# Performance work log

Measured on AMD Instinct MI355X. Metric: run time of the kernel, lower is better.

## Reference

```python
import jax, jax.numpy as jnp
from jax import lax
import numpy as np

B, T, D_IN, H, L, D_OUT = 1024, 512, 6, 128, 3, 1


def _lstm_layer(xs, w_ih, w_hh, b_ih, b_hh):
    """xs: [B, T, Din]; w_ih: [4H, Din]; w_hh: [4H, H]. PyTorch gate order i,f,g,o."""
    Bq = xs.shape[0]
    Hq = w_hh.shape[1]
    # Precompute the input projection for all timesteps (compute-dense part).
    x_proj = jnp.einsum('btd,gd->btg', xs, w_ih) + (b_ih + b_hh)  # [B, T, 4H]

    def step(carry, xp):
        h, c = carry
        gates = xp + h @ w_hh.T  # [B, 4H]
        i, f, g, o = jnp.split(gates, 4, axis=-1)
        i = jax.nn.sigmoid(i)
        f = jax.nn.sigmoid(f)
        g = jnp.tanh(g)
        o = jax.nn.sigmoid(o)
        c = f * c + i * g
        h = o * jnp.tanh(c)
        return (h, c), h

    h0 = jnp.zeros((Bq, Hq), xs.dtype)
    c0 = jnp.zeros((Bq, Hq), xs.dtype)
    (_, _), hs = lax.scan(step, (h0, c0), jnp.swapaxes(x_proj, 0, 1))  # hs: [T, B, H]
    return jnp.swapaxes(hs, 0, 1)  # [B, T, H]


def setup_inputs() -> dict:
    key = jax.random.key(0)
    ks = jax.random.split(key, 16)
    s = 1.0 / np.sqrt(H)  # PyTorch LSTM init scale
    inp = {"x": jax.random.normal(ks[0], (B, T, D_IN), dtype=jnp.float32)}
    din = D_IN
    for l in range(L):
        inp[f"w_ih{l}"] = jax.random.uniform(ks[1 + 4 * l], (4 * H, din), minval=-s, maxval=s, dtype=jnp.float32)
        inp[f"w_hh{l}"] = jax.random.uniform(ks[2 + 4 * l], (4 * H, H), minval=-s, maxval=s, dtype=jnp.float32)
        inp[f"b_ih{l}"] = jax.random.uniform(ks[3 + 4 * l], (4 * H,), minval=-s, maxval=s, dtype=jnp.float32)
        inp[f"b_hh{l}"] = jax.random.uniform(ks[4 + 4 * l], (4 * H,), minval=-s, maxval=s, dtype=jnp.float32)
        din = H
    inp["fc_w"] = jax.random.uniform(ks[13], (D_OUT, H), minval=-s, maxval=s, dtype=jnp.float32)
    inp["fc_b"] = jax.random.uniform(ks[14], (D_OUT,), minval=-s, maxval=s, dtype=jnp.float32)
    return inp


def reference(x, w_ih0, w_hh0, b_ih0, b_hh0, w_ih1, w_hh1, b_ih1, b_hh1,
              w_ih2, w_hh2, b_ih2, b_hh2, fc_w, fc_b):
    # 3-layer LSTM (inference: dropout between layers is identity) + final Linear on last timestep.
    h = _lstm_layer(x, w_ih0, w_hh0, b_ih0, b_hh0)
    h = _lstm_layer(h, w_ih1, w_hh1, b_ih1, b_hh1)
    h = _lstm_layer(h, w_ih2, w_hh2, b_ih2, b_hh2)
    return h[:, -1, :] @ fc_w.T + fc_b  # [B, 1]
```

## Files before the change

kernel.cpp:

```cpp
#include <hip/hip_runtime.h>

#define TLEN  512
#define HID   128
#define RSLOT 16

typedef __attribute__((ext_vector_type(8))) short          bf16x8;
typedef __attribute__((ext_vector_type(4))) float          f32x4;
typedef __attribute__((ext_vector_type(4))) unsigned short u16x4;
typedef unsigned long long u64;

#define LOG2E  1.4426950408889634f
#define LOG2E2 2.8853900817779268f

template<bool B> struct BC { static constexpr bool value = B; };

__device__ __forceinline__ unsigned short f2bf(float f) {
    union { float f; unsigned u; } v; v.f = f;
    unsigned r = v.u + 0x7fffu + ((v.u >> 16) & 1u);
    return (unsigned short)(r >> 16);
}
__device__ __forceinline__ unsigned short f2bf_fast(float f) {
    union { float f; unsigned u; } v; v.f = f;
    return (unsigned short)((v.u + 0x8000u) >> 16);
}

__device__ __forceinline__ float sig_ps(float xs) {
    return __builtin_amdgcn_rcpf(1.0f + __builtin_exp2f(-xs));
}
__device__ __forceinline__ float tanh_ps(float xs) {
    return 2.0f * __builtin_amdgcn_rcpf(1.0f + __builtin_exp2f(-xs)) - 1.0f;
}


__device__ __forceinline__ int flag_peek(const int* f) {
    return __hip_atomic_load(f, __ATOMIC_RELAXED, __HIP_MEMORY_SCOPE_AGENT);
}
__device__ __forceinline__ int flag_spin(const int* f, int v) {
    int x = flag_peek(f);
    while (x < v) { __builtin_amdgcn_s_sleep(1); x = flag_peek(f); }
    return x;
}
__device__ __forceinline__ void flag_pub(int* f, int v) {
    __hip_atomic_store(f, v, __ATOMIC_RELAXED, __HIP_MEMORY_SCOPE_WORKGROUP);
}

template<int MODE, bool CONS, bool PROD, bool WFC>
__device__ __forceinline__ void run_layer_p(
    const float* __restrict__ xin,
    const u64* __restrict__ rin, u64* __restrict__ rout,
    const int* pin_flag, int* cout_flag, const int* cin_flag, int* pout_flag,
    const float* __restrict__ wih, const float* __restrict__ whh,
    const float* __restrict__ bih, const float* __restrict__ bhh,
    unsigned short (* __restrict__ hbuf)[2048],
    unsigned short (* __restrict__ xbuf)[2048],
    float* __restrict__ fcred,
    const int tid, const int wave, const int lane,
    const int n16, const int quad, const int bbase)
{
    constexpr int NKTX = MODE ? 4 : 1;
    constexpr int DINL = MODE ? 128 : 6;

    bf16x8 Wfx[4][NKTX], Wfh[4][4];
    float  bb[4];
#pragma unroll
    for (int g = 0; g < 4; ++g) {
        const float sc = (g == 2) ? LOG2E2 : LOG2E;
        const int row = g * 128 + wave * 16 + n16;
        bb[g] = (bih[row] + bhh[row]) * sc;
#pragma unroll
        for (int kt = 0; kt < NKTX; ++kt) {
            bf16x8 wv;
#pragma unroll
            for (int j = 0; j < 8; ++j) {
                const int k = kt * 32 + quad * 8 + j;
                wv[j] = (short)f2bf(((k < DINL) ? wih[row * DINL + k] : 0.0f) * sc);
            }
            Wfx[g][kt] = wv;
        }
#pragma unroll
        for (int kt = 0; kt < 4; ++kt) {
            bf16x8 wv;
#pragma unroll
            for (int j = 0; j < 8; ++j) {
                const int k = kt * 32 + quad * 8 + j;
                wv[j] = (short)f2bf(whh[row * HID + k] * sc);
            }
            Wfh[g][kt] = wv;
        }
    }

    const int rof  = (lane ^ quad) * 8;
    const int j    = wave * 16 + n16;
    const int beta = ((j & 31) >> 3) & 3;
    const int wbase = ((j >> 5) * 64 + ((j & 31) >> 3) * 16 + quad * 4) * 8 + (j & 7);
    int wof[4];
#pragma unroll
    for (int r = 0; r < 4; ++r) wof[r] = wbase + ((r ^ beta) * 8);
    const int uof  = ((((tid >> 1) ^ ((tid >> 5) & 3))) << 3) + (tid & 1) * 4;
    const int xm = tid >> 5, xk = tid & 31;
    const int eiS = ((xk >> 3) * 16 + (xm ^ (xk >> 3))) * 8 + (xk & 7);

    { u16x4 z = {0, 0, 0, 0}; *(u16x4*)&hbuf[0][uof] = z; }
    u64 q0 = 0, q1 = 0, q2 = 0, qn = 0;
    float pfx0 = 0.0f;
    int pend = 0, cpend = 0;
    if constexpr (CONS) {
        flag_spin(pin_flag, 1);
        *(u64*)&xbuf[0][uof] =
            __hip_atomic_load(rin + tid, __ATOMIC_RELAXED, __HIP_MEMORY_SCOPE_AGENT);
        flag_spin(pin_flag, 2);
        *(u64*)&xbuf[1][uof] =
            __hip_atomic_load(rin + 512 + tid, __ATOMIC_RELAXED, __HIP_MEMORY_SCOPE_AGENT);
        pend = flag_spin(pin_flag, 5);
        q0 = __hip_atomic_load(rin + 2 * 512 + tid, __ATOMIC_RELAXED, __HIP_MEMORY_SCOPE_AGENT);
        q1 = __hip_atomic_load(rin + 3 * 512 + tid, __ATOMIC_RELAXED, __HIP_MEMORY_SCOPE_AGENT);
        q2 = __hip_atomic_load(rin + 4 * 512 + tid, __ATOMIC_RELAXED, __HIP_MEMORY_SCOPE_AGENT);
    } else {
        float v0 = (xk < DINL) ? xin[((bbase + xm) * TLEN + 0) * DINL + xk] : 0.0f;
        float v1 = (xk < DINL) ? xin[((bbase + xm) * TLEN + 1) * DINL + xk] : 0.0f;
        xbuf[0][eiS] = f2bf(v0);
        xbuf[1][eiS] = f2bf(v1);
        if (xk < DINL) pfx0 = xin[((bbase + xm) * TLEN + 2) * DINL + xk];
    }
    if constexpr (PROD) cpend = -(1 << 30);
    __syncthreads();

    f32x4 accA[4], accB[4];
#pragma unroll
    for (int g = 0; g < 4; ++g) { f32x4 bi = {bb[g], bb[g], bb[g], bb[g]}; accA[g] = bi; }
#pragma unroll
    for (int kt = 0; kt < NKTX; ++kt) {
        bf16x8 a = *(const bf16x8*)&xbuf[0][rof + kt * 512];
#pragma unroll
        for (int g = 0; g < 4; ++g)
            accA[g] = __builtin_amdgcn_mfma_f32_16x16x32_bf16(a, Wfx[g][kt], accA[g], 0, 0, 0);
    }

    float cst[4] = {0.f, 0.f, 0.f, 0.f};
    float hf[4];
    int rd = 1, wr = 2;

    auto step = [&](auto SHc, auto CMc, f32x4 (&accC)[4], f32x4 (&accN)[4], int t) {
        constexpr bool SH = decltype(SHc)::value;
        constexpr bool CM = decltype(CMc)::value;
        const int cur = t & 1, nxt = cur ^ 1;
        __syncthreads();

        const unsigned short* __restrict__ hcur = hbuf[cur];
        const unsigned short* __restrict__ xrd  = xbuf[rd];

        bf16x8 ha_[4];
#pragma unroll
        for (int kt = 0; kt < 4; ++kt) ha_[kt] = *(const bf16x8*)&hcur[rof + kt * 512];

        if constexpr (CONS) {
            if (t + 5 < TLEN) {
                if (pend < t + 6) pend = flag_spin(pin_flag, t + 6);
                qn = __hip_atomic_load(rin + ((t + 5) & (RSLOT - 1)) * 512 + tid,
                                       __ATOMIC_RELAXED, __HIP_MEMORY_SCOPE_AGENT);
                pend = flag_peek(pin_flag);
            }
        }
        if (tid == 0) {
            if constexpr (CONS) if ((t & 3) == 0) flag_pub(cout_flag, t + 5);
            if constexpr (PROD) if (t >= 2)       flag_pub(pout_flag, t - 1);
        }
        if constexpr (PROD) {
            if (t >= 1) {
                const int e = t - 1;
                if ((e & 3) == 0 && e + 4 > RSLOT && cpend < e + 4 - RSLOT)
                    cpend = flag_spin(cin_flag, e + 4 - RSLOT);
                u64 hv = *(const u64*)&hcur[uof];
                __hip_atomic_store(rout + (e & (RSLOT - 1)) * 512 + tid, hv,
                                   __ATOMIC_RELAXED, __HIP_MEMORY_SCOPE_WORKGROUP);
                if ((e & 3) == 1) cpend = flag_peek(cin_flag);
            }
        }
        float pfx1 = 0.0f;
        if constexpr (!CONS) {
            if (t + 3 < TLEN && xk < DINL)
                pfx1 = xin[((bbase + xm) * TLEN + (t + 3)) * DINL + xk];
        }

#pragma unroll
        for (int kt = 0; kt < 4; ++kt)
#pragma unroll
            for (int g = 0; g < 4; ++g)
                accC[g] = __builtin_amdgcn_mfma_f32_16x16x32_bf16(ha_[kt], Wfh[g][kt], accC[g], 0, 0, 0);

        bf16x8 xa_[2];
        if constexpr (SH) {
#pragma unroll
            for (int g = 0; g < 4; ++g) { f32x4 bi = {bb[g], bb[g], bb[g], bb[g]}; accN[g] = bi; }
            xa_[0] = *(const bf16x8*)&xrd[rof];
        }
#pragma unroll
        for (int r = 0; r < 4; ++r) {
            if constexpr (SH) {
                if (r + 1 < NKTX)
                    xa_[(r + 1) & 1] = *(const bf16x8*)&xrd[rof + (r + 1) * 512];
            }
            const float iv = sig_ps (accC[0][r]);
            const float fv = sig_ps (accC[1][r]);
            const float gv = tanh_ps(accC[2][r]);
            const float ov = sig_ps (accC[3][r]);
            const float c  = fv * cst[r] + iv * gv;
            cst[r] = c;
            const float h  = ov * tanh_ps(c * LOG2E2);
            if constexpr (WFC) hf[r] = h;
            hbuf[nxt][wof[r]] = f2bf_fast(h);
            if constexpr (SH) {
                if (r < NKTX) {
#pragma unroll
                    for (int g = 0; g < 4; ++g)
                        accN[g] = __builtin_amdgcn_mfma_f32_16x16x32_bf16(xa_[r & 1], Wfx[g][r], accN[g], 0, 0, 0);
                }
            }
        }
        if constexpr (WFC) {
            if (t == TLEN - 1)
#pragma unroll
                for (int r = 0; r < 4; ++r)
                    fcred[(quad * 4 + r) * HID + wave * 16 + n16] = hf[r];
        }
        if constexpr (CM) {
            if constexpr (CONS) {
                *(u64*)&xbuf[wr][uof] = q0;
                q0 = q1; q1 = q2; q2 = qn;
            } else {
                xbuf[wr][eiS] = f2bf(pfx0);
                pfx0 = pfx1;
            }
        }
        rd = wr; wr = (wr == 2) ? 0 : wr + 1;
    };

    for (int t = 0; t < TLEN - 2; t += 2) {
        step(BC<true>{}, BC<true>{}, accA, accB, t);
        step(BC<true>{}, BC<true>{}, accB, accA, t + 1);
    }
    step(BC<true>{},  BC<false>{}, accA, accB, TLEN - 2);
    step(BC<false>{}, BC<false>{}, accB, accA, TLEN - 1);

    if constexpr (PROD) {
        __syncthreads();
        if (tid == 0) flag_pub(pout_flag, TLEN - 1);
        {
            flag_spin(cin_flag, TLEN - RSLOT);
            u64 hv = *(const u64*)&hbuf[TLEN & 1][uof];
            __hip_atomic_store(rout + ((TLEN - 1) & (RSLOT - 1)) * 512 + tid, hv,
                               __ATOMIC_RELAXED, __HIP_MEMORY_SCOPE_WORKGROUP);
        }
        __syncthreads();
        if (tid == 0) flag_pub(pout_flag, TLEN);
    }
}

extern "C" __global__ __launch_bounds__(512, 1)
void lstm3_pipe_kernel(const float* __restrict__ xin,
    const float* __restrict__ wih0, const float* __restrict__ whh0,
    const float* __restrict__ bih0, const float* __restrict__ bhh0,
    const float* __restrict__ wih1, const float* __restrict__ whh1,
    const float* __restrict__ bih1, const float* __restrict__ bhh1,
    const float* __restrict__ wih2, const float* __restrict__ whh2,
    const float* __restrict__ bih2, const float* __restrict__ bhh2,
    const float* __restrict__ fcw, const float* __restrict__ fcb,
    float* __restrict__ out,
    int* __restrict__ flags, u64* __restrict__ ring0, u64* __restrict__ ring1)
{
    __shared__ unsigned short hbuf[2][2048];
    __shared__ unsigned short xbuf[3][2048];
    __shared__ float fcred[16 * HID];

    const int tid   = threadIdx.x;
    const int wave  = tid >> 6;
    const int lane  = tid & 63;
    const int n16   = lane & 15;
    const int quad  = lane >> 4;

    const int xcd    = blockIdx.x & 7;
    const int grp    = blockIdx.x >> 3;
    const int layer  = grp % 3;
    const int sgroup = grp / 3;
    const int slice  = sgroup * 8 + xcd;
    const int bbase  = slice * 16;

    u64* r0 = ring0 + (size_t)slice * (RSLOT * 512);
    u64* r1 = ring1 + (size_t)slice * (RSLOT * 512);
    int* prod0 = flags + (size_t)(0 * 64 + slice) * 64;
    int* prod1 = flags + (size_t)(1 * 64 + slice) * 64;
    int* cons1 = flags + (size_t)(2 * 64 + slice) * 64;
    int* cons2 = flags + (size_t)(3 * 64 + slice) * 64;

    if (layer == 0) {
        run_layer_p<0, false, true, false>(xin, nullptr, r0,
            nullptr, nullptr, cons1, prod0,
            wih0, whh0, bih0, bhh0, hbuf, xbuf, fcred, tid, wave, lane, n16, quad, bbase);
    } else if (layer == 1) {
        run_layer_p<1, true, true, false>(nullptr, r0, r1,
            prod0, cons1, cons2, prod1,
            wih1, whh1, bih1, bhh1, hbuf, xbuf, fcred, tid, wave, lane, n16, quad, bbase);
    } else {
        run_layer_p<1, true, false, true>(nullptr, r1, nullptr,
            prod1, cons2, nullptr, nullptr,
            wih2, whh2, bih2, bhh2, hbuf, xbuf, fcred, tid, wave, lane, n16, quad, bbase);
        __syncthreads();
        if (tid < 16) {
            float s = 0.0f;
#pragma unroll 8
            for (int j = 0; j < HID; ++j) s += fcw[j] * fcred[tid * HID + j];
            out[bbase + tid] = s + fcb[0];
        }
    }
}

extern "C" void kernel_launch(void* const* d_in, const int* in_sizes, int n_in,
                              void* d_out, int out_size, void* d_ws, size_t ws_size,
                              hipStream_t stream) {
    (void)in_sizes; (void)n_in; (void)out_size; (void)ws_size;
    const float* x    = (const float*)d_in[0];
    const float* wih0 = (const float*)d_in[1];
    const float* whh0 = (const float*)d_in[2];
    const float* bih0 = (const float*)d_in[3];
    const float* bhh0 = (const float*)d_in[4];
    const float* wih1 = (const float*)d_in[5];
    const float* whh1 = (const float*)d_in[6];
    const float* bih1 = (const float*)d_in[7];
    const float* bhh1 = (const float*)d_in[8];
    const float* wih2 = (const float*)d_in[9];
    const float* whh2 = (const float*)d_in[10];
    const float* bih2 = (const float*)d_in[11];
    const float* bhh2 = (const float*)d_in[12];
    const float* fcw  = (const float*)d_in[13];
    const float* fcb  = (const float*)d_in[14];
    float* out = (float*)d_out;

    int* flags = (int*)d_ws;
    u64* ring0 = (u64*)((char*)d_ws + 65536);
    u64* ring1 = ring0 + (size_t)64 * RSLOT * 512;

    lstm3_pipe_kernel<<<dim3(192), dim3(512), 0, stream>>>(
        x, wih0, whh0, bih0, bhh0, wih1, whh1, bih1, bhh1,
        wih2, whh2, bih2, bhh2, fcw, fcb, out, flags, ring0, ring1);
}
```

Measured before the change: 813.9 us.

## Merge gate activations into shared reciprocals and unroll steps with constant buffer indices

Rewrites the LSTM cell math so that i*g and o*tanh(c) each use one reciprocal of a product of denominators instead of two, which cuts transcendental ops per element. The cell-state tanh argument is clamped so the product of denominators cannot overflow. The bias is fed as the MFMA accumulator input rather than being copied in with separate moves. The time loop is unrolled by six so the h and x ring-buffer indices become compile-time constants. That unroll raises code size, and the loop bound must line up with the 510 iterations.

```diff
diff --git a/kernel.cpp b/kernel.cpp
--- a/kernel.cpp
+++ b/kernel.cpp
@@ -13,6 +13,7 @@
 #define LOG2E2 2.8853900817779268f
 
 template<bool B> struct BC { static constexpr bool value = B; };
+template<int I>  struct IC { static constexpr int  value = I; };
 
 __device__ __forceinline__ unsigned short f2bf(float f) {
     union { float f; unsigned u; } v; v.f = f;
@@ -22,13 +23,6 @@
 __device__ __forceinline__ unsigned short f2bf_fast(float f) {
     union { float f; unsigned u; } v; v.f = f;
     return (unsigned short)((v.u + 0x8000u) >> 16);
-}
-
-__device__ __forceinline__ float sig_ps(float xs) {
-    return __builtin_amdgcn_rcpf(1.0f + __builtin_exp2f(-xs));
-}
-__device__ __forceinline__ float tanh_ps(float xs) {
-    return 2.0f * __builtin_amdgcn_rcpf(1.0f + __builtin_exp2f(-xs)) - 1.0f;
 }
 
 
@@ -61,12 +55,14 @@
     constexpr int DINL = MODE ? 128 : 6;
 
     bf16x8 Wfx[4][NKTX], Wfh[4][4];
-    float  bb[4];
+    f32x4  bbv[4];
 #pragma unroll
     for (int g = 0; g < 4; ++g) {
         const float sc = (g == 2) ? LOG2E2 : LOG2E;
         const int row = g * 128 + wave * 16 + n16;
-        bb[g] = (bih[row] + bhh[row]) * sc;
+        const float bg = (bih[row] + bhh[row]) * sc;
+        f32x4 bi = {bg, bg, bg, bg};
+        bbv[g] = bi;
 #pragma unroll
         for (int kt = 0; kt < NKTX; ++kt) {
             bf16x8 wv;
@@ -127,27 +123,29 @@
 
     f32x4 accA[4], accB[4];
 #pragma unroll
-    for (int g = 0; g < 4; ++g) { f32x4 bi = {bb[g], bb[g], bb[g], bb[g]}; accA[g] = bi; }
-#pragma unroll
     for (int kt = 0; kt < NKTX; ++kt) {
         bf16x8 a = *(const bf16x8*)&xbuf[0][rof + kt * 512];
 #pragma unroll
         for (int g = 0; g < 4; ++g)
-            accA[g] = __builtin_amdgcn_mfma_f32_16x16x32_bf16(a, Wfx[g][kt], accA[g], 0, 0, 0);
+            accA[g] = __builtin_amdgcn_mfma_f32_16x16x32_bf16(
+                a, Wfx[g][kt], (kt == 0) ? bbv[g] : accA[g], 0, 0, 0);
     }
 
     float cst[4] = {0.f, 0.f, 0.f, 0.f};
     float hf[4];
-    int rd = 1, wr = 2;
-
-    auto step = [&](auto SHc, auto CMc, f32x4 (&accC)[4], f32x4 (&accN)[4], int t) {
-        constexpr bool SH = decltype(SHc)::value;
-        constexpr bool CM = decltype(CMc)::value;
-        const int cur = t & 1, nxt = cur ^ 1;
+
+    auto step = [&](auto SHc, auto CMc, auto CURc, auto RDc, auto WRc,
+                    f32x4 (&accC)[4], f32x4 (&accN)[4], int t) {
+        constexpr bool SH  = decltype(SHc)::value;
+        constexpr bool CM  = decltype(CMc)::value;
+        constexpr int  CUR = decltype(CURc)::value;
+        constexpr int  NXT = CUR ^ 1;
+        constexpr int  RD  = decltype(RDc)::value;
+        constexpr int  WR  = decltype(WRc)::value;
         __syncthreads();
 
-        const unsigned short* __restrict__ hcur = hbuf[cur];
-        const unsigned short* __restrict__ xrd  = xbuf[rd];
+        const unsigned short* __restrict__ hcur = hbuf[CUR];
+        const unsigned short* __restrict__ xrd  = xbuf[RD];
 
         bf16x8 ha_[4];
 #pragma unroll
@@ -189,31 +187,40 @@
                 accC[g] = __builtin_amdgcn_mfma_f32_16x16x32_bf16(ha_[kt], Wfh[g][kt], accC[g], 0, 0, 0);
 
         bf16x8 xa_[2];
-        if constexpr (SH) {
-#pragma unroll
-            for (int g = 0; g < 4; ++g) { f32x4 bi = {bb[g], bb[g], bb[g], bb[g]}; accN[g] = bi; }
-            xa_[0] = *(const bf16x8*)&xrd[rof];
-        }
+        if constexpr (SH) xa_[0] = *(const bf16x8*)&xrd[rof];
 #pragma unroll
         for (int r = 0; r < 4; ++r) {
             if constexpr (SH) {
                 if (r + 1 < NKTX)
                     xa_[(r + 1) & 1] = *(const bf16x8*)&xrd[rof + (r + 1) * 512];
             }
-            const float iv = sig_ps (accC[0][r]);
-            const float fv = sig_ps (accC[1][r]);
-            const float gv = tanh_ps(accC[2][r]);
-            const float ov = sig_ps (accC[3][r]);
-            const float c  = fv * cst[r] + iv * gv;
+            const float An = __builtin_exp2f(-accC[0][r]);
+            const float fv = __builtin_amdgcn_rcpf(1.0f + __builtin_exp2f(-accC[1][r]));
+            const float En = __builtin_exp2f(-accC[2][r]);
+            const float Dn = __builtin_exp2f(-accC[3][r]);
+            const float ig = (1.0f - En) *
+                __builtin_amdgcn_rcpf((1.0f + An) * (1.0f + En));
+            const float c  = fv * cst[r] + ig;
             cst[r] = c;
-            const float h  = ov * tanh_ps(c * LOG2E2);
+            const float xs = fminf(fmaxf(c * LOG2E2, -30.0f), 30.0f);
+            const float Cn = __builtin_exp2f(-xs);
+            const float h  = (1.0f - Cn) *
+                __builtin_amdgcn_rcpf((1.0f + Dn) * (1.0f + Cn));
             if constexpr (WFC) hf[r] = h;
-            hbuf[nxt][wof[r]] = f2bf_fast(h);
+            hbuf[NXT][wof[r]] = f2bf_fast(h);
             if constexpr (SH) {
                 if (r < NKTX) {
-#pragma unroll
-                    for (int g = 0; g < 4; ++g)
-                        accN[g] = __builtin_amdgcn_mfma_f32_16x16x32_bf16(xa_[r & 1], Wfx[g][r], accN[g], 0, 0, 0);
+                    if (r == 0) {
+#pragma unroll
+                        for (int g = 0; g < 4; ++g)
+                            accN[g] = __builtin_amdgcn_mfma_f32_16x16x32_bf16(
+                                xa_[0], Wfx[g][0], bbv[g], 0, 0, 0);
+                    } else {
+#pragma unroll
+                        for (int g = 0; g < 4; ++g)
+                            accN[g] = __builtin_amdgcn_mfma_f32_16x16x32_bf16(
+                                xa_[r & 1], Wfx[g][r], accN[g], 0, 0, 0);
+                    }
                 }
             }
         }
@@ -225,22 +232,25 @@
         }
         if constexpr (CM) {
             if constexpr (CONS) {
-                *(u64*)&xbuf[wr][uof] = q0;
+                *(u64*)&xbuf[WR][uof] = q0;
                 q0 = q1; q1 = q2; q2 = qn;
             } else {
-                xbuf[wr][eiS] = f2bf(pfx0);
+                xbuf[WR][eiS] = f2bf(pfx0);
                 pfx0 = pfx1;
             }
         }
-        rd = wr; wr = (wr == 2) ? 0 : wr + 1;
     };
 
-    for (int t = 0; t < TLEN - 2; t += 2) {
-        step(BC<true>{}, BC<true>{}, accA, accB, t);
-        step(BC<true>{}, BC<true>{}, accB, accA, t + 1);
-    }
-    step(BC<true>{},  BC<false>{}, accA, accB, TLEN - 2);
-    step(BC<false>{}, BC<false>{}, accB, accA, TLEN - 1);
+    for (int t = 0; t < TLEN - 2; t += 6) {
+        step(BC<true>{}, BC<true>{}, IC<0>{}, IC<1>{}, IC<2>{}, accA, accB, t);
+        step(BC<true>{}, BC<true>{}, IC<1>{}, IC<2>{}, IC<0>{}, accB, accA, t + 1);
+        step(BC<true>{}, BC<true>{}, IC<0>{}, IC<0>{}, IC<1>{}, accA, accB, t + 2);
+        step(BC<true>{}, BC<true>{}, IC<1>{}, IC<1>{}, IC<2>{}, accB, accA, t + 3);
+        step(BC<true>{}, BC<true>{}, IC<0>{}, IC<2>{}, IC<0>{}, accA, accB, t + 4);
+        step(BC<true>{}, BC<true>{}, IC<1>{}, IC<0>{}, IC<1>{}, accB, accA, t + 5);
+    }
+    step(BC<true>{},  BC<false>{}, IC<0>{}, IC<1>{}, IC<2>{}, accA, accB, TLEN - 2);
+    step(BC<false>{}, BC<false>{}, IC<1>{}, IC<2>{}, IC<0>{}, accB, accA, TLEN - 1);
 
     if constexpr (PROD) {
         __syncthreads();
```

New measurement: 775.6 us. 4.7% less time.
